# Kernel tuning notes

Hardware: AMD Instinct MI355X
Metric: run time of the kernel (lower is better)

## Reference

```python
import jax, jax.numpy as jnp
import numpy as np

B, C, T, H, W = 8, 256, 16, 28, 28
RED = 2
CR = C // RED
BN_EPS = 1e-5


def conv1x1(x, w, b):
    # x: [b,c,t,h,w], w: [out,c], b: [out] -> [b,out,t,h,w]
    return jnp.einsum('oc,bcthw->bothw', w, x) + b[None, :, None, None, None]


def setup_inputs() -> dict:
    key = jax.random.key(0)
    ks = jax.random.split(key, 12)
    s_in = 1.0 / np.sqrt(C)
    s_cr = 1.0 / np.sqrt(CR)
    return {
        'x': jax.random.normal(ks[0], (B, C, T, H, W), dtype=jnp.float32),
        'Wq': jax.random.normal(ks[1], (CR, C), dtype=jnp.float32) * s_in,
        'bq': jax.random.normal(ks[2], (CR,), dtype=jnp.float32) * 0.01,
        'Wk': jax.random.normal(ks[3], (CR, C), dtype=jnp.float32) * s_in,
        'bk': jax.random.normal(ks[4], (CR,), dtype=jnp.float32) * 0.01,
        'Wv': jax.random.normal(ks[5], (CR, C), dtype=jnp.float32) * s_in,
        'bv': jax.random.normal(ks[6], (CR,), dtype=jnp.float32) * 0.01,
        'Wr': jax.random.normal(ks[7], (C, CR), dtype=jnp.float32) * s_cr,
        'br': jax.random.normal(ks[8], (C,), dtype=jnp.float32) * 0.01,
        'gamma': 1.0 + 0.1 * jax.random.normal(ks[9], (C,), dtype=jnp.float32),
        'beta': 0.1 * jax.random.normal(ks[10], (C,), dtype=jnp.float32),
        'bn_mean': 0.1 * jax.random.normal(ks[11], (C,), dtype=jnp.float32),
        'bn_var': jnp.ones((C,), dtype=jnp.float32),
    }


def reference(x, Wq, bq, Wk, bk, Wv, bv, Wr, br, gamma, beta, bn_mean, bn_var):
    b, c, t, h, w = x.shape
    cr = c // RED
    hw = h * w
    k_top = hw // 4

    Q = conv1x1(x, Wq, bq).reshape(b * cr, t, hw)
    K = conv1x1(x, Wk, bk).reshape(b * cr, t, hw)
    V = conv1x1(x, Wv, bv).reshape(b * cr, t, hw)

    # top-k (descending, sorted) along spatial dim
    Q_tk, _ = jax.lax.top_k(Q, k_top)  # [b*cr, t, k]
    K_tk, _ = jax.lax.top_k(K, k_top)  # [b*cr, t, k]

    corr = jnp.einsum('ntk,nsk->nts', Q_tk, K_tk)  # [b*cr, t, t]
    attn = jax.nn.softmax(corr, axis=-1)
    y = jnp.einsum('nts,nsp->ntp', attn, V)        # [b*cr, t, hw]
    y = y.reshape(b, cr, t, h, w)

    # reconstruct: 1x1 conv + BatchNorm3d (eval-mode with running stats)
    y = conv1x1(y, Wr, br)
    scale = gamma / jnp.sqrt(bn_var + BN_EPS)
    y = y * scale[None, :, None, None, None] + (beta - bn_mean * scale)[None, :, None, None, None]
    return y + x
```

## Files before the change

### kernel.cpp

```cpp
#include <hip/hip_runtime.h>
#include <hip/hip_bf16.h>
#include <cfloat>

#define B_   8
#define C_   256
#define CR_  128
#define T_   16
#define HW_  784
#define THW_ 12544
#define N_   1024
#define KTOP 196

typedef __attribute__((ext_vector_type(8))) short short8;
typedef __attribute__((ext_vector_type(4))) float float4_;

__device__ __forceinline__ unsigned short f2bf(float x) {
    unsigned int u = __float_as_uint(x);
    unsigned int r = u + 0x7fffu + ((u >> 16) & 1u);
    return (unsigned short)(r >> 16);
}
__device__ __forceinline__ float bf2f(unsigned short s) {
    return __uint_as_float(((unsigned int)s) << 16);
}

__global__ __launch_bounds__(256) void prep(
    const float* __restrict__ Wq, const float* __restrict__ Wk,
    const float* __restrict__ Wv, const float* __restrict__ Wr,
    const float* __restrict__ bq, const float* __restrict__ bk,
    const float* __restrict__ bv, const float* __restrict__ br,
    const float* __restrict__ gamma, const float* __restrict__ beta,
    const float* __restrict__ bn_mean, const float* __restrict__ bn_var,
    unsigned short* __restrict__ Whi, unsigned short* __restrict__ Wlo,
    unsigned short* __restrict__ Wrbf, float* __restrict__ bias3,
    float* __restrict__ A1, float* __restrict__ A2)
{
    int idx = blockIdx.x * 256 + threadIdx.x;
    if (idx < 384 * 256) {
        int o = idx >> 8, k = idx & 255;
        int m = o >> 7, r = o & 127;
        const float* W = (m == 0) ? Wq : (m == 1) ? Wk : Wv;
        float v = W[r * 256 + k];
        unsigned short h = f2bf(v);
        Whi[idx] = h;
        Wlo[idx] = f2bf(v - bf2f(h));
    }
    if (idx < 256 * 128) {
        Wrbf[idx] = f2bf(Wr[idx]);
    }
    if (idx < 384) {
        bias3[idx] = (idx < 128) ? bq[idx] : (idx < 256) ? bk[idx - 128] : bv[idx - 256];
    }
    if (idx < 256) {
        float sc = gamma[idx] * rsqrtf(bn_var[idx] + 1e-5f);
        A1[idx] = sc;
        A2[idx] = br[idx] * sc + beta[idx] - bn_mean[idx] * sc;
    }
}

__global__ __launch_bounds__(256) void gemm_qkv_mfma(
    const unsigned short* __restrict__ Whi, const unsigned short* __restrict__ Wlo,
    const float* __restrict__ x, const float* __restrict__ bias3,
    float* __restrict__ Qb, float* __restrict__ Kb, float* __restrict__ Vb)
{
    const int tid  = threadIdx.x;
    const int wave = tid >> 6;
    const int lane = tid & 63;
    const int quad = lane >> 4;
    const int l16  = lane & 15;
    const int p0   = blockIdx.x * 64;
    const int b    = blockIdx.y;
    const int mW   = wave * 96;

    __shared__ unsigned short Ald[2][384][40];

    float4_ acc[6][4];
#pragma unroll
    for (int i = 0; i < 6; i++)
#pragma unroll
        for (int j = 0; j < 4; j++) acc[i][j] = (float4_)0.f;

    const float* xb = x + (size_t)b * C_ * THW_;

    for (int k0 = 0; k0 < 256; k0 += 32) {
#pragma unroll
        for (int var = 0; var < 2; var++) {
            const unsigned short* Wsrc = var ? Wlo : Whi;
#pragma unroll
            for (int it = 0; it < 6; it++) {
                int cc = tid + it * 256;
                int o  = cc >> 2;
                int j  = cc & 3;
                *(uint4*)&Ald[var][o][j * 8] =
                    *(const uint4*)&Wsrc[(size_t)o * 256 + k0 + j * 8];
            }
        }
        __syncthreads();

        short8 Bh[4], Bl[4];
#pragma unroll
        for (int nf = 0; nf < 4; nf++) {
            const float* bp = xb + (size_t)(k0 + quad * 8) * THW_ + p0 + nf * 16 + l16;
#pragma unroll
            for (int jj = 0; jj < 8; jj++) {
                float v = bp[(size_t)jj * THW_];
                unsigned short h = f2bf(v);
                Bh[nf][jj] = (short)h;
                Bl[nf][jj] = (short)f2bf(v - bf2f(h));
            }
        }

#pragma unroll
        for (int mf = 0; mf < 6; mf++) {
            short8 Ah = *(const short8*)&Ald[0][mW + mf * 16 + l16][quad * 8];
            short8 Al = *(const short8*)&Ald[1][mW + mf * 16 + l16][quad * 8];
#pragma unroll
            for (int nf = 0; nf < 4; nf++) {
                acc[mf][nf] = __builtin_amdgcn_mfma_f32_16x16x32_bf16(Al, Bh[nf], acc[mf][nf], 0, 0, 0);
                acc[mf][nf] = __builtin_amdgcn_mfma_f32_16x16x32_bf16(Ah, Bl[nf], acc[mf][nf], 0, 0, 0);
                acc[mf][nf] = __builtin_amdgcn_mfma_f32_16x16x32_bf16(Ah, Bh[nf], acc[mf][nf], 0, 0, 0);
            }
        }
        __syncthreads();
    }

#pragma unroll
    for (int mf = 0; mf < 6; mf++) {
#pragma unroll
        for (int r = 0; r < 4; r++) {
            int oo  = mW + mf * 16 + quad * 4 + r;
            int mat = oo >> 7;
            int cr  = oo & 127;
            float bi = bias3[oo];
            float* dst = ((mat == 0) ? Qb : (mat == 1) ? Kb : Vb)
                         + ((size_t)(b * 128 + cr)) * THW_ + p0 + l16;
#pragma unroll
            for (int nf = 0; nf < 4; nf++)
                dst[nf * 16] = acc[mf][nf][r] + bi;
        }
    }
}

__global__ __launch_bounds__(256) void topk_sort_wave(
    const float* __restrict__ Qb, const float* __restrict__ Kb,
    float* __restrict__ Qtk, float* __restrict__ Ktk)
{
    const int wave = threadIdx.x >> 6;
    const int lane = threadIdx.x & 63;
    const int gw   = blockIdx.x * 4 + wave;
    const int mat  = gw >> 14;
    const int row  = gw & 16383;
    const float* src = ((mat == 0) ? Qb : Kb) + (size_t)row * HW_;
    float* dst       = ((mat == 0) ? Qtk : Ktk) + (size_t)row * KTOP;

    float v[16];
    if (lane < 49) {
        const float4* s4 = (const float4*)(src + lane * 16);
#pragma unroll
        for (int q = 0; q < 4; q++) {
            float4 t = s4[q];
            v[q * 4 + 0] = t.x; v[q * 4 + 1] = t.y;
            v[q * 4 + 2] = t.z; v[q * 4 + 3] = t.w;
        }
    } else {
#pragma unroll
        for (int r = 0; r < 16; r++) v[r] = -FLT_MAX;
    }

#pragma unroll
    for (int k = 2; k <= 1024; k <<= 1) {
#pragma unroll
        for (int j = k >> 1; j >= 1; j >>= 1) {
            if (j >= 16) {
                const int jl = j >> 4;
                const bool up      = ((lane & (k >> 4)) == 0);
                const bool isLower = ((lane & jl) == 0);
                const bool keepMax = (up == isLower);
#pragma unroll
                for (int r = 0; r < 16; r++) {
                    float other = __shfl_xor(v[r], jl, 64);
                    float mx = fmaxf(v[r], other);
                    float mn = fminf(v[r], other);
                    v[r] = keepMax ? mx : mn;
                }
            } else {
#pragma unroll
                for (int r = 0; r < 16; r++) {
                    if ((r & j) == 0) {
                        const int rb = r | j;
                        const bool up = (k >= 16) ? ((lane & (k >> 4)) == 0)
                                                  : ((r & k) == 0);
                        float a = v[r], b = v[rb];
                        float hi = fmaxf(a, b), lo = fminf(a, b);
                        v[r]  = up ? hi : lo;
                        v[rb] = up ? lo : hi;
                    }
                }
            }
        }
    }

    if (lane < 12) {
        float4* d4 = (float4*)(dst + lane * 16);
#pragma unroll
        for (int q = 0; q < 4; q++) {
            float4 t;
            t.x = v[q * 4 + 0]; t.y = v[q * 4 + 1];
            t.z = v[q * 4 + 2]; t.w = v[q * 4 + 3];
            d4[q] = t;
        }
    } else if (lane == 12) {
        float4 t;
        t.x = v[0]; t.y = v[1]; t.z = v[2]; t.w = v[3];
        *(float4*)(dst + 192) = t;
    }
}

__global__ __launch_bounds__(256) void corr_softmax(
    const float* __restrict__ Qtk, const float* __restrict__ Ktk,
    float* __restrict__ attn)
{
    const int n = blockIdx.x;
    __shared__ float qs[T_ * KTOP];
    __shared__ float ks[T_ * KTOP];
    __shared__ float cm[T_][T_ + 1];
    __shared__ float mx[T_], sm[T_];
    const int tid = threadIdx.x;

    for (int i = tid; i < T_ * KTOP; i += 256) {
        qs[i] = Qtk[(size_t)n * T_ * KTOP + i];
        ks[i] = Ktk[(size_t)n * T_ * KTOP + i];
    }
    __syncthreads();

    const int t = tid >> 4, sidx = tid & 15;
    const float* qr = &qs[t * KTOP];
    const float* kr = &ks[sidx * KTOP];
    float c = 0.f;
#pragma unroll 4
    for (int i = 0; i < KTOP; i++) c += qr[i] * kr[i];
    cm[t][sidx] = c;
    __syncthreads();

    if (tid < T_) {
        float m = cm[tid][0];
        for (int i = 1; i < T_; i++) m = fmaxf(m, cm[tid][i]);
        mx[tid] = m;
    }
    __syncthreads();
    float e = expf(c - mx[t]);
    cm[t][sidx] = e;
    __syncthreads();
    if (tid < T_) {
        float ssum = 0.f;
        for (int i = 0; i < T_; i++) ssum += cm[tid][i];
        sm[tid] = ssum;
    }
    __syncthreads();
    attn[(size_t)n * 256 + tid] = e / sm[t];
}

__global__ __launch_bounds__(256) void apply_attn_T(
    const float* __restrict__ attn, const float* __restrict__ V,
    unsigned short* __restrict__ yT)
{
    const int pc = blockIdx.x;
    const int b  = blockIdx.y;
    const int p0 = pc * 16;
    const int tid = threadIdx.x;
    const int crl = tid & 15;
    const int g   = tid >> 4;

    __shared__ float at[16][257];
    __shared__ float vt[16][257];

    for (int chunk = 0; chunk < 8; chunk++) {
        const int crbase = chunk * 16;
        for (int i = tid; i < 16 * 256; i += 256) {
            int cr = i >> 8, ts = i & 255;
            at[cr][ts] = attn[((size_t)(b * 128 + crbase + cr)) * 256 + ts];
        }
        for (int i = tid; i < 16 * 256; i += 256) {
            int cr = i >> 8, s = (i >> 4) & 15, p = i & 15;
            vt[cr][s * 16 + p] =
                V[((size_t)(b * 128 + crbase + cr)) * THW_ + s * HW_ + p0 + p];
        }
        __syncthreads();

        const int cr = crbase + crl;
#pragma unroll
        for (int u = 0; u < 16; u++) {
            int idx = g * 16 + u;
            int t = idx >> 4, p = idx & 15;
            float sum = 0.f;
#pragma unroll
            for (int s = 0; s < 16; s++)
                sum += at[crl][t * 16 + s] * vt[crl][s * 16 + p];
            yT[((size_t)b * THW_ + t * HW_ + p0 + p) * 128 + cr] = f2bf(sum);
        }
        __syncthreads();
    }
}

__global__ __launch_bounds__(256) void gemm_recon_mfma(
    const unsigned short* __restrict__ Wrbf, const unsigned short* __restrict__ yT,
    const float* __restrict__ A1, const float* __restrict__ A2,
    const float* __restrict__ x, float* __restrict__ out)
{
    const int tid  = threadIdx.x;
    const int wave = tid >> 6;
    const int lane = tid & 63;
    const int quad = lane >> 4;
    const int l16  = lane & 15;
    const int p0   = blockIdx.x * 64;
    const int b    = blockIdx.y;
    const int mW   = wave * 64;

    float4_ acc[4][4];
#pragma unroll
    for (int i = 0; i < 4; i++)
#pragma unroll
        for (int j = 0; j < 4; j++) acc[i][j] = (float4_)0.f;

    const unsigned short* yTb = yT + (size_t)b * THW_ * 128;

#pragma unroll
    for (int k0 = 0; k0 < 128; k0 += 32) {
        short8 Bf[4];
#pragma unroll
        for (int nf = 0; nf < 4; nf++)
            Bf[nf] = *(const short8*)&yTb[(size_t)(p0 + nf * 16 + l16) * 128 + k0 + quad * 8];
#pragma unroll
        for (int mf = 0; mf < 4; mf++) {
            short8 Af = *(const short8*)&Wrbf[(size_t)(mW + mf * 16 + l16) * 128 + k0 + quad * 8];
#pragma unroll
            for (int nf = 0; nf < 4; nf++)
                acc[mf][nf] = __builtin_amdgcn_mfma_f32_16x16x32_bf16(Af, Bf[nf], acc[mf][nf], 0, 0, 0);
        }
    }

#pragma unroll
    for (int mf = 0; mf < 4; mf++) {
#pragma unroll
        for (int r = 0; r < 4; r++) {
            int co = mW + mf * 16 + quad * 4 + r;
            float sc = A1[co], sh = A2[co];
            size_t base = ((size_t)b * 256 + co) * THW_ + p0 + l16;
#pragma unroll
            for (int nf = 0; nf < 4; nf++) {
                float xv = x[base + nf * 16];
                out[base + nf * 16] = acc[mf][nf][r] * sc + sh + xv;
            }
        }
    }
}

extern "C" void kernel_launch(void* const* d_in, const int* in_sizes, int n_in,
                              void* d_out, int out_size, void* d_ws, size_t ws_size,
                              hipStream_t stream)
{
    const float* x      = (const float*)d_in[0];
    const float* Wq     = (const float*)d_in[1];
    const float* bq     = (const float*)d_in[2];
    const float* Wk     = (const float*)d_in[3];
    const float* bk     = (const float*)d_in[4];
    const float* Wv     = (const float*)d_in[5];
    const float* bv     = (const float*)d_in[6];
    const float* Wr     = (const float*)d_in[7];
    const float* br     = (const float*)d_in[8];
    const float* gamma  = (const float*)d_in[9];
    const float* beta   = (const float*)d_in[10];
    const float* bn_mean= (const float*)d_in[11];
    const float* bn_var = (const float*)d_in[12];
    float* out = (float*)d_out;

    float* Qb = out;
    float* Kb = out + (size_t)N_ * THW_;

    char* ws = (char*)d_ws;
    float* Vb            = (float*)ws;                       ws += (size_t)N_ * THW_ * 4;
    unsigned short* yT   = (unsigned short*)ws;              ws += (size_t)N_ * THW_ * 2;
    float* Qtk           = (float*)ws;                       ws += (size_t)N_ * T_ * KTOP * 4;
    float* Ktk           = (float*)ws;                       ws += (size_t)N_ * T_ * KTOP * 4;
    float* attn          = (float*)ws;                       ws += (size_t)N_ * T_ * T_ * 4;
    unsigned short* Whi  = (unsigned short*)ws;              ws += 384 * 256 * 2;
    unsigned short* Wlo  = (unsigned short*)ws;              ws += 384 * 256 * 2;
    unsigned short* Wrbf = (unsigned short*)ws;              ws += 256 * 128 * 2;
    float* bias3         = (float*)ws;                       ws += 384 * 4;
    float* A1            = (float*)ws;                       ws += 256 * 4;
    float* A2            = (float*)ws;                       ws += 256 * 4;

    prep<<<dim3(384), 256, 0, stream>>>(Wq, Wk, Wv, Wr, bq, bk, bv, br,
                                        gamma, beta, bn_mean, bn_var,
                                        Whi, Wlo, Wrbf, bias3, A1, A2);
    gemm_qkv_mfma<<<dim3(196, 8), 256, 0, stream>>>(Whi, Wlo, x, bias3, Qb, Kb, Vb);
    topk_sort_wave<<<dim3(8192), 256, 0, stream>>>(Qb, Kb, Qtk, Ktk);
    corr_softmax<<<dim3(1024), 256, 0, stream>>>(Qtk, Ktk, attn);
    apply_attn_T<<<dim3(49, 8), 256, 0, stream>>>(attn, Vb, yT);
    gemm_recon_mfma<<<dim3(196, 8), 256, 0, stream>>>(Wrbf, yT, A1, A2, x, out);
}
```

Measured before the change: 575.3 us.

## Restructure top-k bitonic sort, drop LDS staging in QKV GEMM, tile attention apply

Three separate changes. The QKV GEMM now reads the hi/lo bf16 weight fragments straight from global memory instead of staging them through LDS, which removes two barriers per k-step but relies on L1/L2 to serve the repeated weight reads. The top-k bitonic sort is rewritten as a monotone descending variant that uses reversed-partner merges, fewer selects and ds_swizzle for lane distances up to 31. The attention-apply kernel stores attn transposed and computes a 4x4 register tile per thread with float4 LDS reads, giving more reuse per LDS load.

```diff
diff --git a/kernel.cpp b/kernel.cpp
--- a/kernel.cpp
+++ b/kernel.cpp
@@ -21,6 +21,16 @@
 }
 __device__ __forceinline__ float bf2f(unsigned short s) {
     return __uint_as_float(((unsigned int)s) << 16);
+}
+
+template<int MASK>
+__device__ __forceinline__ float lane_xor_f(float x) {
+    if constexpr (MASK <= 31) {
+        return __int_as_float(__builtin_amdgcn_ds_swizzle(
+            __float_as_int(x), (MASK << 10) | 0x1F));
+    } else {
+        return __shfl_xor(x, MASK, 64);
+    }
 }
 
 __global__ __launch_bounds__(256) void prep(
@@ -71,8 +81,6 @@
     const int b    = blockIdx.y;
     const int mW   = wave * 96;
 
-    __shared__ unsigned short Ald[2][384][40];
-
     float4_ acc[6][4];
 #pragma unroll
     for (int i = 0; i < 6; i++)
@@ -82,20 +90,6 @@
     const float* xb = x + (size_t)b * C_ * THW_;
 
     for (int k0 = 0; k0 < 256; k0 += 32) {
-#pragma unroll
-        for (int var = 0; var < 2; var++) {
-            const unsigned short* Wsrc = var ? Wlo : Whi;
-#pragma unroll
-            for (int it = 0; it < 6; it++) {
-                int cc = tid + it * 256;
-                int o  = cc >> 2;
-                int j  = cc & 3;
-                *(uint4*)&Ald[var][o][j * 8] =
-                    *(const uint4*)&Wsrc[(size_t)o * 256 + k0 + j * 8];
-            }
-        }
-        __syncthreads();
-
         short8 Bh[4], Bl[4];
 #pragma unroll
         for (int nf = 0; nf < 4; nf++) {
@@ -111,8 +105,9 @@
 
 #pragma unroll
         for (int mf = 0; mf < 6; mf++) {
-            short8 Ah = *(const short8*)&Ald[0][mW + mf * 16 + l16][quad * 8];
-            short8 Al = *(const short8*)&Ald[1][mW + mf * 16 + l16][quad * 8];
+            size_t rowoff = (size_t)(mW + mf * 16 + l16) * 256 + k0 + quad * 8;
+            short8 Ah = *(const short8*)&Whi[rowoff];
+            short8 Al = *(const short8*)&Wlo[rowoff];
 #pragma unroll
             for (int nf = 0; nf < 4; nf++) {
                 acc[mf][nf] = __builtin_amdgcn_mfma_f32_16x16x32_bf16(Al, Bh[nf], acc[mf][nf], 0, 0, 0);
@@ -120,7 +115,6 @@
                 acc[mf][nf] = __builtin_amdgcn_mfma_f32_16x16x32_bf16(Ah, Bh[nf], acc[mf][nf], 0, 0, 0);
             }
         }
-        __syncthreads();
     }
 
 #pragma unroll
@@ -140,6 +134,55 @@
     }
 }
 
+template<int J>
+__device__ __forceinline__ void cross_steps(float v[16], int lane) {
+    if constexpr (J >= 16) {
+        constexpr int JL = J >> 4;
+        const bool kj = (lane & JL) == 0;
+        float t[16];
+#pragma unroll
+        for (int r = 0; r < 16; r++) t[r] = lane_xor_f<JL>(v[r]);
+#pragma unroll
+        for (int r = 0; r < 16; r++) {
+            float mx = fmaxf(v[r], t[r]), mn = fminf(v[r], t[r]);
+            v[r] = kj ? mx : mn;
+        }
+        cross_steps<J / 2>(v, lane);
+    }
+}
+
+__device__ __forceinline__ void inreg_steps(float v[16], int jmax) {
+#pragma unroll
+    for (int j = 8; j >= 1; j >>= 1) {
+        if (j > jmax) continue;
+#pragma unroll
+        for (int r = 0; r < 16; r++) {
+            if ((r & j) == 0) {
+                int rp = r | j;
+                float a = v[r], b2 = v[rp];
+                v[r]  = fmaxf(a, b2);
+                v[rp] = fminf(a, b2);
+            }
+        }
+    }
+}
+
+template<int K>
+__device__ __forceinline__ void stage_ge32(float v[16], int lane) {
+    constexpr int LM = (K - 1) >> 4;
+    const bool km = (lane & (K >> 5)) == 0;
+    float t[16];
+#pragma unroll
+    for (int r = 0; r < 16; r++) t[r] = lane_xor_f<LM>(v[15 - r]);
+#pragma unroll
+    for (int r = 0; r < 16; r++) {
+        float mx = fmaxf(v[r], t[r]), mn = fminf(v[r], t[r]);
+        v[r] = km ? mx : mn;
+    }
+    cross_steps<K / 4>(v, lane);
+    inreg_steps(v, 8);
+}
+
 __global__ __launch_bounds__(256) void topk_sort_wave(
     const float* __restrict__ Qb, const float* __restrict__ Kb,
     float* __restrict__ Qtk, float* __restrict__ Ktk)
@@ -167,37 +210,37 @@
     }
 
 #pragma unroll
-    for (int k = 2; k <= 1024; k <<= 1) {
-#pragma unroll
-        for (int j = k >> 1; j >= 1; j >>= 1) {
-            if (j >= 16) {
-                const int jl = j >> 4;
-                const bool up      = ((lane & (k >> 4)) == 0);
-                const bool isLower = ((lane & jl) == 0);
-                const bool keepMax = (up == isLower);
-#pragma unroll
-                for (int r = 0; r < 16; r++) {
-                    float other = __shfl_xor(v[r], jl, 64);
-                    float mx = fmaxf(v[r], other);
-                    float mn = fminf(v[r], other);
-                    v[r] = keepMax ? mx : mn;
+    for (int k = 2; k <= 16; k <<= 1) {
+#pragma unroll
+        for (int r = 0; r < 16; r++) {
+            if ((r & (k >> 1)) == 0) {
+                int rp = r ^ (k - 1);
+                float a = v[r], b2 = v[rp];
+                v[r]  = fmaxf(a, b2);
+                v[rp] = fminf(a, b2);
+            }
+        }
+#pragma unroll
+        for (int j = 8; j >= 1; j >>= 1) {
+            if (j > (k >> 2)) continue;
+#pragma unroll
+            for (int r = 0; r < 16; r++) {
+                if ((r & j) == 0) {
+                    int rp = r | j;
+                    float a = v[r], b2 = v[rp];
+                    v[r]  = fmaxf(a, b2);
+                    v[rp] = fminf(a, b2);
                 }
-            } else {
-#pragma unroll
-                for (int r = 0; r < 16; r++) {
-                    if ((r & j) == 0) {
-                        const int rb = r | j;
-                        const bool up = (k >= 16) ? ((lane & (k >> 4)) == 0)
-                                                  : ((r & k) == 0);
-                        float a = v[r], b = v[rb];
-                        float hi = fmaxf(a, b), lo = fminf(a, b);
-                        v[r]  = up ? hi : lo;
-                        v[rb] = up ? lo : hi;
-                    }
-                }
-            }
-        }
-    }
+            }
+        }
+    }
+
+    stage_ge32<32>(v, lane);
+    stage_ge32<64>(v, lane);
+    stage_ge32<128>(v, lane);
+    stage_ge32<256>(v, lane);
+    stage_ge32<512>(v, lane);
+    stage_ge32<1024>(v, lane);
 
     if (lane < 12) {
         float4* d4 = (float4*)(dst + lane * 16);
@@ -269,34 +312,51 @@
     const int tid = threadIdx.x;
     const int crl = tid & 15;
     const int g   = tid >> 4;
-
-    __shared__ float at[16][257];
-    __shared__ float vt[16][257];
+    const int t0  = (g & 3) * 4;
+    const int pl0 = (g >> 2) * 4;
+
+    __shared__ float atT[16][264];
+    __shared__ float vt[16][264];
 
     for (int chunk = 0; chunk < 8; chunk++) {
         const int crbase = chunk * 16;
-        for (int i = tid; i < 16 * 256; i += 256) {
-            int cr = i >> 8, ts = i & 255;
-            at[cr][ts] = attn[((size_t)(b * 128 + crbase + cr)) * 256 + ts];
-        }
-        for (int i = tid; i < 16 * 256; i += 256) {
+        for (int i = tid; i < 4096; i += 256) {
+            int cr = i >> 8, t = (i >> 4) & 15, s = i & 15;
+            atT[cr][s * 16 + t] =
+                attn[((size_t)(b * 128 + crbase + cr)) * 256 + t * 16 + s];
+        }
+        for (int i = tid; i < 4096; i += 256) {
             int cr = i >> 8, s = (i >> 4) & 15, p = i & 15;
             vt[cr][s * 16 + p] =
                 V[((size_t)(b * 128 + crbase + cr)) * THW_ + s * HW_ + p0 + p];
         }
         __syncthreads();
 
+        float acc[4][4];
+#pragma unroll
+        for (int i = 0; i < 4; i++)
+#pragma unroll
+            for (int j = 0; j < 4; j++) acc[i][j] = 0.f;
+
+#pragma unroll
+        for (int s = 0; s < 16; s++) {
+            float4 av = *(const float4*)&atT[crl][s * 16 + t0];
+            float4 vv = *(const float4*)&vt[crl][s * 16 + pl0];
+            float a0 = av.x, a1 = av.y, a2 = av.z, a3 = av.w;
+            float b0 = vv.x, b1 = vv.y, b2 = vv.z, b3 = vv.w;
+            acc[0][0] += a0 * b0; acc[0][1] += a0 * b1; acc[0][2] += a0 * b2; acc[0][3] += a0 * b3;
+            acc[1][0] += a1 * b0; acc[1][1] += a1 * b1; acc[1][2] += a1 * b2; acc[1][3] += a1 * b3;
+            acc[2][0] += a2 * b0; acc[2][1] += a2 * b1; acc[2][2] += a2 * b2; acc[2][3] += a2 * b3;
+            acc[3][0] += a3 * b0; acc[3][1] += a3 * b1; acc[3][2] += a3 * b2; acc[3][3] += a3 * b3;
+        }
+
         const int cr = crbase + crl;
 #pragma unroll
-        for (int u = 0; u < 16; u++) {
-            int idx = g * 16 + u;
-            int t = idx >> 4, p = idx & 15;
-            float sum = 0.f;
-#pragma unroll
-            for (int s = 0; s < 16; s++)
-                sum += at[crl][t * 16 + s] * vt[crl][s * 16 + p];
-            yT[((size_t)b * THW_ + t * HW_ + p0 + p) * 128 + cr] = f2bf(sum);
-        }
+        for (int ti = 0; ti < 4; ti++)
+#pragma unroll
+            for (int pi = 0; pi < 4; pi++)
+                yT[((size_t)b * THW_ + (t0 + ti) * HW_ + p0 + pl0 + pi) * 128 + cr]
+                    = f2bf(acc[ti][pi]);
         __syncthreads();
     }
 }
```

Result: slower. 587.1 us (+2.1%).
